# Kernel tuning notes

Hardware: AMD Instinct MI355X
Metric: run time of the kernel (lower is better)

The kernel has to match this reference:

```python
import jax, jax.numpy as jnp
import numpy as np

# Model dims (match init_kwargs)
E, D, H, K = 8, 512, 1024, 2   # num_experts, input/output dim, hidden dim, top_k
B, S = 4, 2048                 # batch, seq_len


def setup_inputs() -> dict:
    key = jax.random.key(0)
    ks = jax.random.split(key, 5)
    sd = lambda fan: np.float32(1.0 / np.sqrt(fan))
    return {
        "x": jax.random.normal(ks[0], (B, S, D), jnp.float32),
        "gate_w": jax.random.normal(ks[1], (D, E), jnp.float32) * sd(D),
        "gate_b": jnp.zeros((E,), jnp.float32),
        "w1": jax.random.normal(ks[2], (E, D, H), jnp.float32) * sd(D),
        "b1": jnp.zeros((E, H), jnp.float32),
        "w2": jax.random.normal(ks[3], (E, H, D), jnp.float32) * sd(H),
        "b2": jnp.zeros((E, D), jnp.float32),
    }


def reference(x, gate_w, gate_b, w1, b1, w2, b2):
    # x: [B, S, D]
    Bb, Ss, Dd = x.shape
    xf = x.reshape(-1, Dd)                              # [N, D], N = B*S

    # Router: softmax over experts, top-k, renormalize selected weights
    logits = xf @ gate_w + gate_b                        # [N, E]
    probs = jax.nn.softmax(logits, axis=-1)              # [N, E]
    top_w, top_i = jax.lax.top_k(probs, K)               # [N, K]
    top_w = top_w / top_w.sum(axis=-1, keepdims=True)

    # Per-token combine weight for each expert (0 if not routed).
    onehot = jax.nn.one_hot(top_i, E, dtype=probs.dtype)  # [N, K, E]
    combine = jnp.einsum("nke,nk->ne", onehot, top_w)     # [N, E]

    # Expert MLPs. Dropout is inactive at inference (identity).
    # h: [E, N, H]; GELU exact (torch nn.GELU default uses erf)
    h = jax.nn.gelu(jnp.einsum("nd,edh->enh", xf, w1) + b1[:, None, :],
                    approximate=False)
    y = jnp.einsum("enh,ehd->end", h, w2) + b2[:, None, :]  # [E, N, D]

    # Weighted combine: tokens not routed to expert e have combine[:, e] == 0.
    out = jnp.einsum("end,ne->nd", y, combine).reshape(Bb, Ss, Dd)
    return out, probs.reshape(Bb, Ss, E)
```

## Files before the change

### kernel.cpp

```cpp
#include <hip/hip_runtime.h>
#include <stdint.h>

#define N_TOK 8192
#define DIM   512
#define HID   1024
#define NE    8
#define NSLOT 16384
#define MAXSLOT 17408

typedef __attribute__((ext_vector_type(8))) short short8;
typedef __attribute__((ext_vector_type(4))) float f32x4;

#define W1T_OFF  0ull
#define W2T_OFF  8388608ull
#define H_OFF    16777216ull
#define Y_OFF    52428800ull
#define XBF_OFF  52428800ull
#define TOPI_OFF 70254592ull
#define TOPW_OFF 70320128ull
#define SLOT_OFF 70385664ull
#define ROWS_OFF 70451200ull
#define RW_OFF   70520832ull
#define CNT_OFF  70590464ull

__device__ __forceinline__ unsigned int f2bfu(float f) {
  union { float f; unsigned int i; } v; v.f = f;
  unsigned int u = v.i;
  return (u + 0x7FFFu + ((u >> 16) & 1u)) >> 16;
}
__device__ __forceinline__ float bf2f(unsigned int u) {
  union { unsigned int i; float f; } v; v.i = (u & 0xFFFFu) << 16; return v.f;
}
__device__ __forceinline__ float gelu_f(float x) {
  float x2 = x * x;
  float u = x * (1.59576912f + 0.07135481f * x2);
  float ez = __expf(-u);
  return x * __builtin_amdgcn_rcpf(1.0f + ez);
}
__device__ __forceinline__ void async16(void* lds, const void* g) {
  __builtin_amdgcn_global_load_lds(
      (const __attribute__((address_space(1))) unsigned int*)g,
      (__attribute__((address_space(3))) unsigned int*)lds, 16, 0, 0);
}

__global__ __launch_bounds__(256) void k_prep(
    const float* __restrict__ w1, const float* __restrict__ w2,
    unsigned short* __restrict__ w1t, unsigned short* __restrict__ w2t,
    const float* __restrict__ x, const float* __restrict__ gw,
    const float* __restrict__ gb, float* __restrict__ probs_out,
    int2* __restrict__ topi, float2* __restrict__ topw,
    unsigned short* __restrict__ xbf) {
  __shared__ unsigned short tile[64][68];
  int b = blockIdx.x, tid = threadIdx.x;
  if (b >= 2048) {
    int wave = tid >> 6, lane = tid & 63;
    int n = (b - 2048) * 4 + wave;
    const float4* xr = (const float4*)(x + (size_t)n * DIM);
    float4 x0 = xr[lane * 2], x1 = xr[lane * 2 + 1];
    float xf[8] = {x0.x, x0.y, x0.z, x0.w, x1.x, x1.y, x1.z, x1.w};
    uint4 pa;
    pa.x = f2bfu(xf[0]) | (f2bfu(xf[1]) << 16);
    pa.y = f2bfu(xf[2]) | (f2bfu(xf[3]) << 16);
    pa.z = f2bfu(xf[4]) | (f2bfu(xf[5]) << 16);
    pa.w = f2bfu(xf[6]) | (f2bfu(xf[7]) << 16);
    *(uint4*)(xbf + (size_t)n * DIM + lane * 8) = pa;
    float acc[8] = {0.f,0.f,0.f,0.f,0.f,0.f,0.f,0.f};
    const float4* gwr = (const float4*)gw;
#pragma unroll
    for (int j = 0; j < 8; ++j) {
      int d = lane * 8 + j;
      float4 g0 = gwr[d * 2], g1 = gwr[d * 2 + 1];
      acc[0] += xf[j] * g0.x; acc[1] += xf[j] * g0.y; acc[2] += xf[j] * g0.z; acc[3] += xf[j] * g0.w;
      acc[4] += xf[j] * g1.x; acc[5] += xf[j] * g1.y; acc[6] += xf[j] * g1.z; acc[7] += xf[j] * g1.w;
    }
#pragma unroll
    for (int o = 1; o < 64; o <<= 1)
#pragma unroll
      for (int e = 0; e < 8; ++e) acc[e] += __shfl_xor(acc[e], o, 64);
    float p[8], mx = -1e30f, s = 0.f;
#pragma unroll
    for (int e = 0; e < 8; ++e) { p[e] = acc[e] + gb[e]; mx = fmaxf(mx, p[e]); }
#pragma unroll
    for (int e = 0; e < 8; ++e) { p[e] = __expf(p[e] - mx); s += p[e]; }
    float inv = 1.f / s;
#pragma unroll
    for (int e = 0; e < 8; ++e) p[e] *= inv;
    if (lane < 8) probs_out[(size_t)n * NE + lane] = p[lane];
    if (lane == 0) {
      int i0 = 0; float v0 = p[0];
#pragma unroll
      for (int e = 1; e < 8; ++e) if (p[e] > v0) { v0 = p[e]; i0 = e; }
      int i1 = -1; float v1 = -1.f;
#pragma unroll
      for (int e = 0; e < 8; ++e) if (e != i0 && p[e] > v1) { v1 = p[e]; i1 = e; }
      float sw = 1.f / (v0 + v1);
      topi[n] = make_int2(i0, i1);
      topw[n] = make_float2(v0 * sw, v1 * sw);
    }
    return;
  }
  const float* src; unsigned short* dst; int R, C;
  if (b < 1024) { int e = b >> 7; int t = b & 127;
    src = w1 + (size_t)e * 524288; dst = w1t + (size_t)e * 524288; R = 512; C = 1024;
    int tr = t >> 4, tc = t & 15;
    src += (size_t)tr * 64 * C + tc * 64; dst += (size_t)tc * 64 * R + tr * 64;
  } else { b -= 1024; int e = b >> 7; int t = b & 127;
    src = w2 + (size_t)e * 524288; dst = w2t + (size_t)e * 524288; R = 1024; C = 512;
    int tr = t >> 3, tc = t & 7;
    src += (size_t)tr * 64 * C + tc * 64; dst += (size_t)tc * 64 * R + tr * 64;
  }
#pragma unroll
  for (int i = 0; i < 4; ++i) {
    int l = i * 256 + tid;
    int r = l >> 4, c4 = (l & 15) << 2;
    float4 v = *(const float4*)(src + (size_t)r * C + c4);
    tile[r][c4 + 0] = (unsigned short)f2bfu(v.x);
    tile[r][c4 + 1] = (unsigned short)f2bfu(v.y);
    tile[r][c4 + 2] = (unsigned short)f2bfu(v.z);
    tile[r][c4 + 3] = (unsigned short)f2bfu(v.w);
  }
  __syncthreads();
#pragma unroll
  for (int i = 0; i < 2; ++i) {
    int l = i * 256 + tid;
    int rr = l >> 3, c8 = (l & 7) << 3;
    ushort4 a, b2v;
    a.x = tile[c8 + 0][rr]; a.y = tile[c8 + 1][rr];
    a.z = tile[c8 + 2][rr]; a.w = tile[c8 + 3][rr];
    b2v.x = tile[c8 + 4][rr]; b2v.y = tile[c8 + 5][rr];
    b2v.z = tile[c8 + 6][rr]; b2v.w = tile[c8 + 7][rr];
    uint4 pk;
    pk.x = (unsigned int)a.x | ((unsigned int)a.y << 16);
    pk.y = (unsigned int)a.z | ((unsigned int)a.w << 16);
    pk.z = (unsigned int)b2v.x | ((unsigned int)b2v.y << 16);
    pk.w = (unsigned int)b2v.z | ((unsigned int)b2v.w << 16);
    *(uint4*)(dst + (size_t)rr * R + c8) = pk;
  }
}

__global__ __launch_bounds__(1024) void k_count(
    const int2* __restrict__ topi, int* __restrict__ meta, int* __restrict__ chunk_base,
    int* __restrict__ rows, float* __restrict__ rw) {
  __shared__ int ch[32][8];
  __shared__ int tot[8], poff_s[9], tiles_s[8];
  int t = threadIdx.x;
  int g = t >> 5;
  if (t < 256) ((int*)ch)[t] = 0;
  __syncthreads();
  int c[8] = {0,0,0,0,0,0,0,0};
  int base_tok = t * 8;
#pragma unroll
  for (int i = 0; i < 8; ++i) {
    int2 e = topi[base_tok + i];
#pragma unroll
    for (int k = 0; k < 8; ++k) c[k] += (e.x == k) + (e.y == k);
  }
#pragma unroll
  for (int k = 0; k < 8; ++k) if (c[k]) atomicAdd(&ch[g][k], c[k]);
  __syncthreads();
  if (t < 8) {
    int a = 0;
#pragma unroll
    for (int b = 0; b < 32; ++b) { int v = ch[b][t]; ch[b][t] = a; a += v; }
    tot[t] = a; meta[t] = a;
  }
  __syncthreads();
  if (t == 0) {
    int a = 0, ts = 0;
#pragma unroll
    for (int e = 0; e < 8; ++e) {
      int tiles = (tot[e] + 127) >> 7;
      poff_s[e] = a; tiles_s[e] = tiles;
      meta[16 + e] = a; meta[32 + e] = ts;
      a += tiles << 7; ts += tiles;
    }
    poff_s[8] = a; meta[24] = a; meta[40] = ts;
  }
  __syncthreads();
  if (t < 256) {
    int b = t >> 3, e = t & 7;
    chunk_base[t] = poff_s[e] + ch[b][e];
  }
#pragma unroll
  for (int e = 0; e < 8; ++e) {
    int padn = (tiles_s[e] << 7) - tot[e];
    if (t < padn) {
      int s = poff_s[e] + tot[e] + t;
      rows[s] = 0; rw[s] = 0.f;
    }
  }
}

__global__ __launch_bounds__(256) void k_assign(
    const int2* __restrict__ topi, const float2* __restrict__ topw,
    const int* __restrict__ chunk_base,
    int* __restrict__ rows, float* __restrict__ rw, int* __restrict__ slot_of) {
  __shared__ int lcnt[8];
  __shared__ int lbase[8];
  int t = threadIdx.x, b = blockIdx.x;
  if (t < 8) { lcnt[t] = 0; lbase[t] = chunk_base[b * 8 + t]; }
  __syncthreads();
  int n = b * 256 + t;
  int2 ei = topi[n]; float2 wv = topw[n];
  int r0 = atomicAdd(&lcnt[ei.x], 1);
  int r1 = atomicAdd(&lcnt[ei.y], 1);
  int s0 = lbase[ei.x] + r0;
  int s1 = lbase[ei.y] + r1;
  rows[s0] = n; rw[s0] = wv.x; slot_of[2 * n] = s0;
  rows[s1] = n; rw[s1] = wv.y; slot_of[2 * n + 1] = s1;
}

__global__ __launch_bounds__(256) void k_gemm1(
    const unsigned short* __restrict__ xbf, const unsigned short* __restrict__ w1t,
    const float* __restrict__ b1, const int* __restrict__ meta,
    const int* __restrict__ rows, unsigned short* __restrict__ h) {
  int t = blockIdx.y;
  if (t >= meta[40]) return;
  int e = 0;
#pragma unroll
  for (int i = 1; i < 8; ++i) if (t >= meta[32 + i]) e = i;
  int mt = t - meta[32 + e];
  int row0 = meta[16 + e] + (mt << 7);
  int nt = blockIdx.x;
  __shared__ __align__(16) unsigned short As[2][8192];
  __shared__ __align__(16) unsigned short Bs[2][8192];
  int tid = threadIdx.x;
  int wave = tid >> 6, lane = tid & 63;
  int wr = wave & 1, wc = wave >> 1;
  f32x4 acc[4][4] = {};
  const unsigned short* bBase = w1t + (size_t)e * HID * DIM + (size_t)(nt * 128) * DIM;

  const unsigned short* ga[4]; const unsigned short* gb[4];
#pragma unroll
  for (int j = 0; j < 4; ++j) {
    int s = j * 256 + tid;
    int r = s >> 3;
    int cg = ((s & 7) ^ (r & 7)) << 3;
    ga[j] = xbf + (size_t)rows[row0 + r] * DIM + cg;
    gb[j] = bBase + (size_t)r * DIM + cg;
  }
  int ldst = (wave * 64) * 8;

#pragma unroll
  for (int j = 0; j < 4; ++j) {
    async16(&As[0][j * 2048 + ldst], ga[j]);
    async16(&Bs[0][j * 2048 + ldst], gb[j]);
  }
  __syncthreads();

  for (int k0 = 0; k0 < DIM; k0 += 64) {
    int cur = (k0 >> 6) & 1, nxt = cur ^ 1;
    if (k0 + 64 < DIM) {
#pragma unroll
      for (int j = 0; j < 4; ++j) {
        async16(&As[nxt][j * 2048 + ldst], ga[j] + k0 + 64);
        async16(&Bs[nxt][j * 2048 + ldst], gb[j] + k0 + 64);
      }
    }
#pragma unroll
    for (int kk = 0; kk < 2; ++kk) {
      int ca = kk * 4 + (lane >> 4);
      short8 tf[4], wf[4];
#pragma unroll
      for (int am = 0; am < 4; ++am) {
        int ra = wr * 64 + am * 16 + (lane & 15);
        tf[am] = *(const short8*)&As[cur][(ra * 8 + (ca ^ (ra & 7))) * 8];
      }
#pragma unroll
      for (int an = 0; an < 4; ++an) {
        int rb = wc * 64 + an * 16 + (lane & 15);
        wf[an] = *(const short8*)&Bs[cur][(rb * 8 + (ca ^ (rb & 7))) * 8];
      }
#pragma unroll
      for (int an = 0; an < 4; ++an)
#pragma unroll
        for (int am = 0; am < 4; ++am)
          acc[an][am] = __builtin_amdgcn_mfma_f32_16x16x32_bf16(wf[an], tf[am], acc[an][am], 0, 0, 0);
    }
    __syncthreads();
  }
  int ml = lane & 15, q = lane >> 4;
#pragma unroll
  for (int am = 0; am < 4; ++am) {
    int slot_r = row0 + wr * 64 + am * 16 + ml;
    unsigned short* hrow = h + (size_t)slot_r * HID;
#pragma unroll
    for (int an = 0; an < 4; ++an) {
      int colb = nt * 128 + wc * 64 + an * 16 + q * 4;
      float4 bias = *(const float4*)&b1[e * HID + colb];
      f32x4 v = acc[an][am];
      float g0 = gelu_f(v[0] + bias.x);
      float g1 = gelu_f(v[1] + bias.y);
      float g2 = gelu_f(v[2] + bias.z);
      float g3 = gelu_f(v[3] + bias.w);
      uint2 pk;
      pk.x = f2bfu(g0) | (f2bfu(g1) << 16);
      pk.y = f2bfu(g2) | (f2bfu(g3) << 16);
      *(uint2*)(hrow + colb) = pk;
    }
  }
}

__global__ __launch_bounds__(256) void k_gemm2(
    const unsigned short* __restrict__ h, const unsigned short* __restrict__ w2t,
    const float* __restrict__ b2, const int* __restrict__ meta,
    const float* __restrict__ rw, unsigned short* __restrict__ y) {
  int t = blockIdx.y;
  if (t >= meta[40]) return;
  int e = 0;
#pragma unroll
  for (int i = 1; i < 8; ++i) if (t >= meta[32 + i]) e = i;
  int mt = t - meta[32 + e];
  int row0 = meta[16 + e] + (mt << 7);
  int nt = blockIdx.x;
  __shared__ __align__(16) unsigned short As[2][8192];
  __shared__ __align__(16) unsigned short Bs[2][4096];
  int tid = threadIdx.x;
  int wave = tid >> 6, lane = tid & 63;
  f32x4 acc[4][2] = {};
  const unsigned short* aBase = h + (size_t)row0 * HID;
  const unsigned short* bBase = w2t + (size_t)e * DIM * HID + (size_t)(nt * 64) * HID;

  const unsigned short* ga[4]; const unsigned short* gb[2];
#pragma unroll
  for (int j = 0; j < 4; ++j) {
    int s = j * 256 + tid;
    int r = s >> 3;
    int cg = ((s & 7) ^ (r & 7)) << 3;
    ga[j] = aBase + (size_t)r * HID + cg;
  }
#pragma unroll
  for (int j = 0; j < 2; ++j) {
    int s = j * 256 + tid;
    int r = s >> 3;
    int cg = ((s & 7) ^ (r & 7)) << 3;
    gb[j] = bBase + (size_t)r * HID + cg;
  }
  int ldst = (wave * 64) * 8;

#pragma unroll
  for (int j = 0; j < 4; ++j) async16(&As[0][j * 2048 + ldst], ga[j]);
#pragma unroll
  for (int j = 0; j < 2; ++j) async16(&Bs[0][j * 2048 + ldst], gb[j]);
  __syncthreads();

  for (int k0 = 0; k0 < HID; k0 += 64) {
    int cur = (k0 >> 6) & 1, nxt = cur ^ 1;
    if (k0 + 64 < HID) {
#pragma unroll
      for (int j = 0; j < 4; ++j) async16(&As[nxt][j * 2048 + ldst], ga[j] + k0 + 64);
#pragma unroll
      for (int j = 0; j < 2; ++j) async16(&Bs[nxt][j * 2048 + ldst], gb[j] + k0 + 64);
    }
#pragma unroll
    for (int kk = 0; kk < 2; ++kk) {
      int ca = kk * 4 + (lane >> 4);
      short8 tf[2], wf[4];
#pragma unroll
      for (int am = 0; am < 2; ++am) {
        int ra = wave * 32 + am * 16 + (lane & 15);
        tf[am] = *(const short8*)&As[cur][(ra * 8 + (ca ^ (ra & 7))) * 8];
      }
#pragma unroll
      for (int an = 0; an < 4; ++an) {
        int rb = an * 16 + (lane & 15);
        wf[an] = *(const short8*)&Bs[cur][(rb * 8 + (ca ^ (rb & 7))) * 8];
      }
#pragma unroll
      for (int an = 0; an < 4; ++an)
#pragma unroll
        for (int am = 0; am < 2; ++am)
          acc[an][am] = __builtin_amdgcn_mfma_f32_16x16x32_bf16(wf[an], tf[am], acc[an][am], 0, 0, 0);
    }
    __syncthreads();
  }
  int ml = lane & 15, q = lane >> 4;
#pragma unroll
  for (int am = 0; am < 2; ++am) {
    int slot_r = row0 + wave * 32 + am * 16 + ml;
    float w = rw[slot_r];
    unsigned short* yrow = y + (size_t)slot_r * DIM;
#pragma unroll
    for (int an = 0; an < 4; ++an) {
      int colb = nt * 64 + an * 16 + q * 4;
      float4 bias = *(const float4*)&b2[e * DIM + colb];
      f32x4 v = acc[an][am];
      uint2 pk;
      pk.x = f2bfu((v[0] + bias.x) * w) | (f2bfu((v[1] + bias.y) * w) << 16);
      pk.y = f2bfu((v[2] + bias.z) * w) | (f2bfu((v[3] + bias.w) * w) << 16);
      *(uint2*)(yrow + colb) = pk;
    }
  }
}

__global__ __launch_bounds__(256) void k_combine(
    const unsigned short* __restrict__ y, const int* __restrict__ slot_of,
    float* __restrict__ out) {
  int t = blockIdx.x * 256 + threadIdx.x;
  int n = t >> 6, c = (t & 63) << 3;
  int s0 = slot_of[2 * n], s1 = slot_of[2 * n + 1];
  uint4 u0 = *(const uint4*)(y + (size_t)s0 * DIM + c);
  uint4 u1 = *(const uint4*)(y + (size_t)s1 * DIM + c);
  float4 o0, o1;
  o0.x = bf2f(u0.x) + bf2f(u1.x); o0.y = bf2f(u0.x >> 16) + bf2f(u1.x >> 16);
  o0.z = bf2f(u0.y) + bf2f(u1.y); o0.w = bf2f(u0.y >> 16) + bf2f(u1.y >> 16);
  o1.x = bf2f(u0.z) + bf2f(u1.z); o1.y = bf2f(u0.z >> 16) + bf2f(u1.z >> 16);
  o1.z = bf2f(u0.w) + bf2f(u1.w); o1.w = bf2f(u0.w >> 16) + bf2f(u1.w >> 16);
  *(float4*)(out + (size_t)n * DIM + c) = o0;
  *(float4*)(out + (size_t)n * DIM + c + 4) = o1;
}

extern "C" void kernel_launch(void* const* d_in, const int* in_sizes, int n_in,
                              void* d_out, int out_size, void* d_ws, size_t ws_size,
                              hipStream_t stream) {
  const float* x  = (const float*)d_in[0];
  const float* gw = (const float*)d_in[1];
  const float* gb = (const float*)d_in[2];
  const float* w1 = (const float*)d_in[3];
  const float* b1 = (const float*)d_in[4];
  const float* w2 = (const float*)d_in[5];
  const float* b2 = (const float*)d_in[6];
  float* out = (float*)d_out;
  char* ws = (char*)d_ws;

  unsigned short* w1t = (unsigned short*)(ws + W1T_OFF);
  unsigned short* w2t = (unsigned short*)(ws + W2T_OFF);
  unsigned short* h   = (unsigned short*)(ws + H_OFF);
  unsigned short* y   = (unsigned short*)(ws + Y_OFF);
  unsigned short* xbf = (unsigned short*)(ws + XBF_OFF);
  int2*   topi    = (int2*)(ws + TOPI_OFF);
  float2* topw    = (float2*)(ws + TOPW_OFF);
  int*    slot_of = (int*)(ws + SLOT_OFF);
  int*    rows    = (int*)(ws + ROWS_OFF);
  float*  rw      = (float*)(ws + RW_OFF);
  int*    meta    = (int*)(ws + CNT_OFF);
  int*    chunk_base = meta + 64;
  float*  probs   = out + (size_t)N_TOK * DIM;

  k_prep   <<<dim3(4096), dim3(256), 0, stream>>>(w1, w2, w1t, w2t,
                                                  x, gw, gb, probs, topi, topw, xbf);
  k_count  <<<dim3(1),    dim3(1024), 0, stream>>>(topi, meta, chunk_base, rows, rw);
  k_assign <<<dim3(32),   dim3(256), 0, stream>>>(topi, topw, chunk_base, rows, rw, slot_of);
  k_gemm1  <<<dim3(8, 136), dim3(256), 0, stream>>>(xbf, w1t, b1, meta, rows, h);
  k_gemm2  <<<dim3(8, 136), dim3(256), 0, stream>>>(h, w2t, b2, meta, rw, y);
  k_combine<<<dim3(2048), dim3(256), 0, stream>>>(y, slot_of, out);
}
```

Measured before the change: 219.7 us.

## Drop LDS staging in expert GEMMs and load MFMA fragments straight from global

Both grouped GEMM kernels stop staging A/B tiles in double-buffered shared memory via async global-to-LDS loads. Each wave now reads its MFMA operand fragments directly from global memory (relying on L1/L2 for reuse), with no barriers. gemm2 also moves to a 128x128 tile with 4x4 accumulators per wave and half the grid width. This removes LDS traffic and synchronisation but gives up cross-wave data sharing, so global/cache bandwidth and load latency become the exposed cost.

```diff
diff --git a/kernel.cpp b/kernel.cpp
--- a/kernel.cpp
+++ b/kernel.cpp
@@ -36,11 +36,6 @@
   float u = x * (1.59576912f + 0.07135481f * x2);
   float ez = __expf(-u);
   return x * __builtin_amdgcn_rcpf(1.0f + ez);
-}
-__device__ __forceinline__ void async16(void* lds, const void* g) {
-  __builtin_amdgcn_global_load_lds(
-      (const __attribute__((address_space(1))) unsigned int*)g,
-      (__attribute__((address_space(3))) unsigned int*)lds, 16, 0, 0);
 }
 
 __global__ __launch_bounds__(256) void k_prep(
@@ -222,64 +217,40 @@
   int mt = t - meta[32 + e];
   int row0 = meta[16 + e] + (mt << 7);
   int nt = blockIdx.x;
-  __shared__ __align__(16) unsigned short As[2][8192];
-  __shared__ __align__(16) unsigned short Bs[2][8192];
   int tid = threadIdx.x;
   int wave = tid >> 6, lane = tid & 63;
   int wr = wave & 1, wc = wave >> 1;
+  int ml = lane & 15, q = lane >> 4;
   f32x4 acc[4][4] = {};
-  const unsigned short* bBase = w1t + (size_t)e * HID * DIM + (size_t)(nt * 128) * DIM;
-
-  const unsigned short* ga[4]; const unsigned short* gb[4];
-#pragma unroll
-  for (int j = 0; j < 4; ++j) {
-    int s = j * 256 + tid;
-    int r = s >> 3;
-    int cg = ((s & 7) ^ (r & 7)) << 3;
-    ga[j] = xbf + (size_t)rows[row0 + r] * DIM + cg;
-    gb[j] = bBase + (size_t)r * DIM + cg;
-  }
-  int ldst = (wave * 64) * 8;
-
-#pragma unroll
-  for (int j = 0; j < 4; ++j) {
-    async16(&As[0][j * 2048 + ldst], ga[j]);
-    async16(&Bs[0][j * 2048 + ldst], gb[j]);
-  }
-  __syncthreads();
-
-  for (int k0 = 0; k0 < DIM; k0 += 64) {
-    int cur = (k0 >> 6) & 1, nxt = cur ^ 1;
-    if (k0 + 64 < DIM) {
-#pragma unroll
-      for (int j = 0; j < 4; ++j) {
-        async16(&As[nxt][j * 2048 + ldst], ga[j] + k0 + 64);
-        async16(&Bs[nxt][j * 2048 + ldst], gb[j] + k0 + 64);
-      }
-    }
-#pragma unroll
-    for (int kk = 0; kk < 2; ++kk) {
-      int ca = kk * 4 + (lane >> 4);
-      short8 tf[4], wf[4];
-#pragma unroll
-      for (int am = 0; am < 4; ++am) {
-        int ra = wr * 64 + am * 16 + (lane & 15);
-        tf[am] = *(const short8*)&As[cur][(ra * 8 + (ca ^ (ra & 7))) * 8];
-      }
-#pragma unroll
-      for (int an = 0; an < 4; ++an) {
-        int rb = wc * 64 + an * 16 + (lane & 15);
-        wf[an] = *(const short8*)&Bs[cur][(rb * 8 + (ca ^ (rb & 7))) * 8];
-      }
-#pragma unroll
-      for (int an = 0; an < 4; ++an)
-#pragma unroll
-        for (int am = 0; am < 4; ++am)
-          acc[an][am] = __builtin_amdgcn_mfma_f32_16x16x32_bf16(wf[an], tf[am], acc[an][am], 0, 0, 0);
-    }
-    __syncthreads();
-  }
-  int ml = lane & 15, q = lane >> 4;
+
+  const unsigned short* abase[4];
+#pragma unroll
+  for (int am = 0; am < 4; ++am) {
+    int ra = wr * 64 + am * 16 + ml;
+    abase[am] = xbf + (size_t)rows[row0 + ra] * DIM + q * 8;
+  }
+  const unsigned short* bbase[4];
+  const unsigned short* wslice = w1t + (size_t)e * HID * DIM + (size_t)(nt * 128) * DIM;
+#pragma unroll
+  for (int an = 0; an < 4; ++an) {
+    int rb = an * 16 + ml;
+    bbase[an] = wslice + (size_t)(wc * 64 + rb) * DIM + q * 8;
+  }
+
+#pragma unroll 4
+  for (int step = 0; step < 16; ++step) {
+    short8 tf[4], wf[4];
+#pragma unroll
+    for (int am = 0; am < 4; ++am) tf[am] = *(const short8*)(abase[am] + step * 32);
+#pragma unroll
+    for (int an = 0; an < 4; ++an) wf[an] = *(const short8*)(bbase[an] + step * 32);
+#pragma unroll
+    for (int an = 0; an < 4; ++an)
+#pragma unroll
+      for (int am = 0; am < 4; ++am)
+        acc[an][am] = __builtin_amdgcn_mfma_f32_16x16x32_bf16(wf[an], tf[am], acc[an][am], 0, 0, 0);
+  }
+
 #pragma unroll
   for (int am = 0; am < 4; ++am) {
     int slot_r = row0 + wr * 64 + am * 16 + ml;
@@ -313,76 +284,49 @@
   int mt = t - meta[32 + e];
   int row0 = meta[16 + e] + (mt << 7);
   int nt = blockIdx.x;
-  __shared__ __align__(16) unsigned short As[2][8192];
-  __shared__ __align__(16) unsigned short Bs[2][4096];
   int tid = threadIdx.x;
   int wave = tid >> 6, lane = tid & 63;
-  f32x4 acc[4][2] = {};
-  const unsigned short* aBase = h + (size_t)row0 * HID;
-  const unsigned short* bBase = w2t + (size_t)e * DIM * HID + (size_t)(nt * 64) * HID;
-
-  const unsigned short* ga[4]; const unsigned short* gb[2];
-#pragma unroll
-  for (int j = 0; j < 4; ++j) {
-    int s = j * 256 + tid;
-    int r = s >> 3;
-    int cg = ((s & 7) ^ (r & 7)) << 3;
-    ga[j] = aBase + (size_t)r * HID + cg;
-  }
-#pragma unroll
-  for (int j = 0; j < 2; ++j) {
-    int s = j * 256 + tid;
-    int r = s >> 3;
-    int cg = ((s & 7) ^ (r & 7)) << 3;
-    gb[j] = bBase + (size_t)r * HID + cg;
-  }
-  int ldst = (wave * 64) * 8;
-
-#pragma unroll
-  for (int j = 0; j < 4; ++j) async16(&As[0][j * 2048 + ldst], ga[j]);
-#pragma unroll
-  for (int j = 0; j < 2; ++j) async16(&Bs[0][j * 2048 + ldst], gb[j]);
-  __syncthreads();
-
-  for (int k0 = 0; k0 < HID; k0 += 64) {
-    int cur = (k0 >> 6) & 1, nxt = cur ^ 1;
-    if (k0 + 64 < HID) {
-#pragma unroll
-      for (int j = 0; j < 4; ++j) async16(&As[nxt][j * 2048 + ldst], ga[j] + k0 + 64);
-#pragma unroll
-      for (int j = 0; j < 2; ++j) async16(&Bs[nxt][j * 2048 + ldst], gb[j] + k0 + 64);
-    }
-#pragma unroll
-    for (int kk = 0; kk < 2; ++kk) {
-      int ca = kk * 4 + (lane >> 4);
-      short8 tf[2], wf[4];
-#pragma unroll
-      for (int am = 0; am < 2; ++am) {
-        int ra = wave * 32 + am * 16 + (lane & 15);
-        tf[am] = *(const short8*)&As[cur][(ra * 8 + (ca ^ (ra & 7))) * 8];
-      }
-#pragma unroll
-      for (int an = 0; an < 4; ++an) {
-        int rb = an * 16 + (lane & 15);
-        wf[an] = *(const short8*)&Bs[cur][(rb * 8 + (ca ^ (rb & 7))) * 8];
-      }
-#pragma unroll
-      for (int an = 0; an < 4; ++an)
-#pragma unroll
-        for (int am = 0; am < 2; ++am)
-          acc[an][am] = __builtin_amdgcn_mfma_f32_16x16x32_bf16(wf[an], tf[am], acc[an][am], 0, 0, 0);
-    }
-    __syncthreads();
-  }
+  int wr = wave & 1, wc = wave >> 1;
   int ml = lane & 15, q = lane >> 4;
-#pragma unroll
-  for (int am = 0; am < 2; ++am) {
-    int slot_r = row0 + wave * 32 + am * 16 + ml;
+  f32x4 acc[4][4] = {};
+
+  const unsigned short* abase[4];
+#pragma unroll
+  for (int am = 0; am < 4; ++am) {
+    int ra = wr * 64 + am * 16 + ml;
+    abase[am] = h + (size_t)(row0 + ra) * HID + q * 8;
+  }
+  const unsigned short* bbase[4];
+  const unsigned short* wslice = w2t + (size_t)e * DIM * HID + (size_t)(nt * 128) * HID;
+#pragma unroll
+  for (int an = 0; an < 4; ++an) {
+    int rb = an * 16 + ml;
+    bbase[an] = wslice + (size_t)(wc * 64 + rb) * HID + q * 8;
+  }
+
+#pragma unroll 4
+  for (int step = 0; step < 32; ++step) {
+    short8 tf[4], wf[4];
+#pragma unroll
+    for (int am = 0; am < 4; ++am) tf[am] = *(const short8*)(abase[am] + step * 32);
+#pragma unroll
+    for (int an = 0; an < 4; ++an) wf[an] = *(const short8*)(bbase[an] + step * 32);
+#pragma unroll
+    for (int an = 0; an < 4; ++an)
+#pragma unroll
+      for (int am = 0; am < 4; ++am)
+        acc[an][am] = __builtin_amdgcn_mfma_f32_16x16x32_bf16(wf[an], tf[am], acc[an][am], 0, 0, 0);
+  }
+
+  int mlq = lane & 15, qq = lane >> 4;
+#pragma unroll
+  for (int am = 0; am < 4; ++am) {
+    int slot_r = row0 + wr * 64 + am * 16 + mlq;
     float w = rw[slot_r];
     unsigned short* yrow = y + (size_t)slot_r * DIM;
 #pragma unroll
     for (int an = 0; an < 4; ++an) {
-      int colb = nt * 64 + an * 16 + q * 4;
+      int colb = nt * 128 + wc * 64 + an * 16 + qq * 4;
       float4 bias = *(const float4*)&b2[e * DIM + colb];
       f32x4 v = acc[an][am];
       uint2 pk;
@@ -442,6 +386,6 @@
   k_count  <<<dim3(1),    dim3(1024), 0, stream>>>(topi, meta, chunk_base, rows, rw);
   k_assign <<<dim3(32),   dim3(256), 0, stream>>>(topi, topw, chunk_base, rows, rw, slot_of);
   k_gemm1  <<<dim3(8, 136), dim3(256), 0, stream>>>(xbf, w1t, b1, meta, rows, h);
-  k_gemm2  <<<dim3(8, 136), dim3(256), 0, stream>>>(h, w2t, b2, meta, rw, y);
+  k_gemm2  <<<dim3(4, 136), dim3(256), 0, stream>>>(h, w2t, b2, meta, rw, y);
   k_combine<<<dim3(2048), dim3(256), 0, stream>>>(y, slot_of, out);
 }
```

Measured after the change: 309.4 us. 1.41x slower.
